# Kernel tuning notes

Hardware: AMD Instinct MI355X
Metric: run time of the kernel (lower is better)

Reference implementation:

```python
import jax, jax.numpy as jnp
import numpy as np

DIM = 512          # model dim
K = 4              # max_block_size (depthwise conv kernel size)
DS = 4             # downsample_factor
BLOCKS = (1, 2, 3, 4)  # block sizes, all offset 0
MULT = 12          # lcm(1,2,3,4) = block_pad_multiple
VOCAB = 256


def setup_inputs() -> dict:
    key = jax.random.key(0)
    ks = jax.random.split(key, 7)
    x = jax.random.randint(ks[0], (4, 4096), 0, VOCAB)
    emb = jax.random.normal(ks[1], (VOCAB, DIM), dtype=jnp.float32) * 0.02
    dw_w = jax.random.normal(ks[2], (DIM, 1, K), dtype=jnp.float32) * 0.1   # depthwise conv weight [out, in/groups, k]
    dw_b = jnp.zeros((DIM,), dtype=jnp.float32)
    pw_w = jax.random.normal(ks[3], (DIM, DIM), dtype=jnp.float32) * 0.05   # 1x1 conv weight [out, in]
    pw_b = jnp.zeros((DIM,), dtype=jnp.float32)
    score_w = jax.random.normal(ks[4], (DIM,), dtype=jnp.float32) * 0.05    # Linear(dim,1)
    score_b = jnp.zeros((), dtype=jnp.float32)
    return {"x": x, "emb": emb, "dw_w": dw_w, "dw_b": dw_b,
            "pw_w": pw_w, "pw_b": pw_b, "score_w": score_w, "score_b": score_b}


def _gbst(x, emb, dw_w, dw_b, pw_w, pw_b, score_w, score_b):
    b, n = x.shape
    m = ((n + DS - 1) // DS) * DS  # next multiple of downsample factor
    xe = emb[x]  # [b, n, d]

    # positional: Pad seq end by K-1, depthwise conv1d(k=K), then 1x1 conv
    xp = jnp.pad(xe, ((0, 0), (0, K - 1), (0, 0)))
    xc = jnp.transpose(xp, (0, 2, 1))  # [b, d, n+K-1]
    y = jax.lax.conv_general_dilated(
        xc, dw_w, window_strides=(1,), padding='VALID',
        dimension_numbers=('NCH', 'OIH', 'NCH'), feature_group_count=DIM)
    y = y + dw_b[None, :, None]                       # [b, d, n]
    y = jnp.einsum('ed,bdn->bne', pw_w, y) + pw_b     # [b, n, d]

    # pad seq to multiple of lcm of block sizes
    L = ((n + MULT - 1) // MULT) * MULT
    xpad = jnp.pad(y, ((0, 0), (0, L - n), (0, 0)))   # [b, L, d]

    # multi-scale block mean pooling, broadcast back to full length
    reprs = []
    for bs in BLOCKS:
        br = xpad.reshape(b, L // bs, bs, DIM).mean(axis=2)  # [b, L/bs, d]
        reprs.append(jnp.repeat(br, bs, axis=1))             # [b, L, d]
    block_reprs = jnp.stack(reprs, axis=2)  # [b, L, nblocks, d]

    # learned block scoring + softmax over block sizes
    scores = jnp.einsum('blkd,d->blk', block_reprs, score_w) + score_b
    scores = jax.nn.softmax(scores, axis=2)  # [b, L, nblocks]

    # consensus attention over positions (inner dim = nblocks)
    sim = jnp.einsum('bik,bjk->bij', scores, scores)  # [b, L, L]
    attn = jax.nn.softmax(sim, axis=-1)
    scores = jnp.einsum('bij,bjk->bik', attn, scores)

    out = jnp.einsum('blkd,blk->bld', block_reprs, scores)  # [b, L, d]
    out = out[:, :m]
    out = out.reshape(b, m // DS, DS, DIM).mean(axis=2)     # [b, m/DS, d]
    return out


def reference(x, emb, dw_w, dw_b, pw_w, pw_b, score_w, score_b):
    return _gbst(x, emb, dw_w, dw_b, pw_w, pw_b, score_w, score_b)
```

## Files before the change

kernel.cpp:

```cpp
#include <hip/hip_runtime.h>
#include <hip/hip_bf16.h>

#define DIMD 512
#define NSEQ 4096
#define LPAD 4104
#define NCH 12
#define CH 342
#define SPLITS 8
#define PT_BK 32

#define OFF_P      0u
#define OFF_CONST  524288u
#define OFF_Q      524800u
#define OFF_S      525824u
#define OFF_AACC   591488u
#define OFF_PPART  657152u

__global__ __launch_bounds__(256) void k_ptable(
    const float* __restrict__ emb, const float* __restrict__ dw_w,
    const float* __restrict__ pw_w, float* __restrict__ Ppart) {
  __shared__ float As[PT_BK][68];
  __shared__ float Bs[PT_BK][68];
  const int tid = threadIdx.x;
  const int m0 = blockIdx.x * 64;
  const int e0 = blockIdx.y * 64;
  const int z  = blockIdx.z;
  const int kk = m0 >> 8;
  const int v0 = m0 & 255;
  const int srow = tid >> 3;
  const int sd4  = (tid & 7) * 4;
  const int ty = tid >> 4, tx = tid & 15;
  float c[4][4] = {};
  for (int kt = 0; kt < 64; kt += PT_BK) {
    const int d0 = z * 64 + kt;
    const float dw0 = dw_w[(d0 + sd4 + 0) * 4 + kk];
    const float dw1 = dw_w[(d0 + sd4 + 1) * 4 + kk];
    const float dw2 = dw_w[(d0 + sd4 + 2) * 4 + kk];
    const float dw3 = dw_w[(d0 + sd4 + 3) * 4 + kk];
    #pragma unroll
    for (int rr = 0; rr < 2; ++rr) {
      const int row = srow + rr * 32;
      float4 ev = *reinterpret_cast<const float4*>(&emb[(v0 + row) * DIMD + d0 + sd4]);
      As[sd4 + 0][row] = ev.x * dw0;
      As[sd4 + 1][row] = ev.y * dw1;
      As[sd4 + 2][row] = ev.z * dw2;
      As[sd4 + 3][row] = ev.w * dw3;
      float4 bv = *reinterpret_cast<const float4*>(&pw_w[(e0 + row) * DIMD + d0 + sd4]);
      Bs[sd4 + 0][row] = bv.x;
      Bs[sd4 + 1][row] = bv.y;
      Bs[sd4 + 2][row] = bv.z;
      Bs[sd4 + 3][row] = bv.w;
    }
    __syncthreads();
    #pragma unroll
    for (int q = 0; q < PT_BK; ++q) {
      float4 a = *reinterpret_cast<const float4*>(&As[q][ty * 4]);
      float4 b = *reinterpret_cast<const float4*>(&Bs[q][tx * 4]);
      c[0][0] += a.x * b.x; c[0][1] += a.x * b.y; c[0][2] += a.x * b.z; c[0][3] += a.x * b.w;
      c[1][0] += a.y * b.x; c[1][1] += a.y * b.y; c[1][2] += a.y * b.z; c[1][3] += a.y * b.w;
      c[2][0] += a.z * b.x; c[2][1] += a.z * b.y; c[2][2] += a.z * b.z; c[2][3] += a.z * b.w;
      c[3][0] += a.w * b.x; c[3][1] += a.w * b.y; c[3][2] += a.w * b.z; c[3][3] += a.w * b.w;
    }
    __syncthreads();
  }
  #pragma unroll
  for (int i = 0; i < 4; ++i) {
    *reinterpret_cast<float4*>(
        &Ppart[(size_t)z * 524288u + (m0 + ty * 4 + i) * DIMD + e0 + tx * 4]) =
        make_float4(c[i][0], c[i][1], c[i][2], c[i][3]);
  }
}

__global__ __launch_bounds__(256) void k_pcomb(
    const float* __restrict__ Ppart, float* __restrict__ P,
    const float* __restrict__ pw_w, const float* __restrict__ pw_b,
    const float* __restrict__ dw_b, const float* __restrict__ score_w,
    float* __restrict__ constv, float* __restrict__ q) {
  __shared__ float qred[4];
  const int tid = threadIdx.x;
  const int idx = blockIdx.x * 256 + tid;
  const float4* p4 = reinterpret_cast<const float4*>(Ppart);
  float4 a = p4[idx];
  #pragma unroll
  for (int zz = 1; zz < SPLITS; ++zz) {
    float4 v = p4[(size_t)zz * 131072u + idx];
    a.x += v.x; a.y += v.y; a.z += v.z; a.w += v.w;
  }
  reinterpret_cast<float4*>(P)[idx] = a;
  float4 sw = reinterpret_cast<const float4*>(score_w)[idx & 127];
  float part = a.x * sw.x + a.y * sw.y + a.z * sw.z + a.w * sw.w;
  for (int off = 32; off > 0; off >>= 1) part += __shfl_down(part, off);
  if ((tid & 63) == 0) qred[tid >> 6] = part;
  __syncthreads();
  if (tid == 0)   q[blockIdx.x * 2 + 0] = qred[0] + qred[1];
  if (tid == 128) q[blockIdx.x * 2 + 1] = qred[2] + qred[3];
  if (blockIdx.x < 2) {
    const int e = blockIdx.x * 256 + tid;
    float acc = pw_b[e];
    const float4* pr = reinterpret_cast<const float4*>(&pw_w[e * DIMD]);
    const float4* db = reinterpret_cast<const float4*>(dw_b);
    for (int d4 = 0; d4 < DIMD / 4; ++d4) {
      float4 w = pr[d4]; float4 bb = db[d4];
      acc += w.x * bb.x + w.y * bb.y + w.z * bb.z + w.w * bb.w;
    }
    constv[e] = acc;
  }
}

__global__ __launch_bounds__(256) void k_scores(
    const int* __restrict__ x, const float* __restrict__ q,
    const float* __restrict__ constv, const float* __restrict__ score_w,
    const float* __restrict__ score_b_p, float* __restrict__ s,
    float* __restrict__ Aacc) {
  __shared__ float qlds[1024];
  __shared__ float tlds[264];
  __shared__ float c0red[2];
  const int b = blockIdx.y;
  const int l0 = blockIdx.x * 256;
  const int tid = threadIdx.x;
  reinterpret_cast<float4*>(qlds)[tid] = reinterpret_cast<const float4*>(q)[tid];
  if (tid < 128) {
    float4 cv = reinterpret_cast<const float4*>(constv)[tid];
    float4 sw = reinterpret_cast<const float4*>(score_w)[tid];
    float part = cv.x * sw.x + cv.y * sw.y + cv.z * sw.z + cv.w * sw.w;
    for (int off = 32; off > 0; off >>= 1) part += __shfl_down(part, off);
    if ((tid & 63) == 0) c0red[tid >> 6] = part;
  }
  __syncthreads();
  const float c0 = c0red[0] + c0red[1];
  const int* xb = &x[b * NSEQ];
  auto tval = [&](int l) -> float {
    if ((unsigned)l >= (unsigned)NSEQ) return 0.f;
    float acc = c0;
    #pragma unroll
    for (int k = 0; k < 4; ++k) {
      const int pos = l + k;
      if (pos < NSEQ) acc += qlds[(k << 8) + xb[pos]];
    }
    return acc;
  };
  tlds[tid] = tval(l0 - 2 + tid);
  if (tid < 5) tlds[256 + tid] = tval(l0 + 254 + tid);
  __syncthreads();
  const int l = l0 + tid;
  if (l >= LPAD) return;
  reinterpret_cast<float4*>(Aacc)[(size_t)(b * LPAD) + l] = make_float4(0.f, 0.f, 0.f, 0.f);
  const float sb = score_b_p[0];
  #define TT(j) tlds[(j) - l0 + 2]
  float p0 = TT(l) + sb;
  int j2 = l & ~1;
  float p1 = (TT(j2) + TT(j2 + 1)) * 0.5f + sb;
  int j3 = (l / 3) * 3;
  float p2 = (TT(j3) + TT(j3 + 1) + TT(j3 + 2)) * (1.0f / 3.0f) + sb;
  int j4 = l & ~3;
  float p3 = (TT(j4) + TT(j4 + 1) + TT(j4 + 2) + TT(j4 + 3)) * 0.25f + sb;
  #undef TT
  float mx = fmaxf(fmaxf(p0, p1), fmaxf(p2, p3));
  float e0 = __expf(p0 - mx), e1 = __expf(p1 - mx);
  float e2 = __expf(p2 - mx), e3 = __expf(p3 - mx);
  float inv = 1.0f / (e0 + e1 + e2 + e3);
  *reinterpret_cast<float4*>(&s[((size_t)(b * LPAD) + l) * 4]) =
      make_float4(e0 * inv, e1 * inv, e2 * inv, e3 * inv);
}

__global__ __launch_bounds__(256) void k_attn(
    const float* __restrict__ s, float* __restrict__ Aacc) {
  const int b = blockIdx.z;
  const int c = blockIdx.y;
  const int i = blockIdx.x * 256 + threadIdx.x;
  __shared__ float4 sch[CH];
  const float4* s4 = reinterpret_cast<const float4*>(s) + (size_t)b * LPAD;
  float4 si = s4[i < LPAD ? i : 0];
  const int j0 = c * CH;
  for (int idx = threadIdx.x; idx < CH; idx += 256) sch[idx] = s4[j0 + idx];
  __syncthreads();
  if (i >= LPAD) return;
  float a0x = 0.f, a0y = 0.f, a0z = 0.f, a0w = 0.f;
  float a1x = 0.f, a1y = 0.f, a1z = 0.f, a1w = 0.f;
  #pragma unroll 3
  for (int jj = 0; jj < CH; jj += 2) {
    float4 u = sch[jj];
    float4 v = sch[jj + 1];
    float d0 = si.x * u.x + si.y * u.y + si.z * u.z + si.w * u.w;
    float d1 = si.x * v.x + si.y * v.y + si.z * v.z + si.w * v.w;
    float e0 = __expf(d0), e1 = __expf(d1);
    a0x += e0 * u.x; a0y += e0 * u.y; a0z += e0 * u.z; a0w += e0 * u.w;
    a1x += e1 * v.x; a1y += e1 * v.y; a1z += e1 * v.z; a1w += e1 * v.w;
  }
  float* aa = &Aacc[((size_t)(b * LPAD) + i) * 4];
  atomicAdd(aa + 0, a0x + a1x);
  atomicAdd(aa + 1, a0y + a1y);
  atomicAdd(aa + 2, a0z + a1z);
  atomicAdd(aa + 3, a0w + a1w);
}

__global__ __launch_bounds__(256) void k_out(
    const int* __restrict__ x, const float* __restrict__ P,
    const float* __restrict__ constv, const float* __restrict__ Aacc,
    float* __restrict__ out) {
  const int b = blockIdx.y;
  const int h = threadIdx.x >> 7;
  const int tl = threadIdx.x & 127;
  const int g = blockIdx.x * 2 + h;
  __shared__ float coef[2][8];
  const int jbase = (g == 0) ? 0 : 4 * g - 2;
  if (tl == 0) {
    float cf[8] = {0.f, 0.f, 0.f, 0.f, 0.f, 0.f, 0.f, 0.f};
    const float4* a4 = reinterpret_cast<const float4*>(Aacc) + (size_t)b * LPAD;
    for (int dl = 0; dl < 4; ++dl) {
      int l = 4 * g + dl;
      float4 av = a4[l];
      float inv = 1.0f / (av.x + av.y + av.z + av.w);
      float sk[4] = {av.x * inv, av.y * inv, av.z * inv, av.w * inv};
      for (int k = 0; k < 4; ++k) {
        int bs = k + 1;
        int j0 = (l / bs) * bs;
        float wv = sk[k] / (float)(bs * 4);
        for (int jj = 0; jj < bs; ++jj) cf[j0 + jj - jbase] += wv;
      }
    }
    for (int r = 0; r < 8; ++r) coef[h][r] = cf[r];
  }
  __syncthreads();
  const int* xb = &x[b * NSEQ];
  float ax = 0.f, ay = 0.f, az = 0.f, aw = 0.f;
  float csum = 0.f;
  #pragma unroll
  for (int r = 0; r < 8; ++r) {
    const int row = jbase + r;
    if (row < NSEQ) {
      const float cr = coef[h][r];
      csum += cr;
      #pragma unroll
      for (int k = 0; k < 4; ++k) {
        const int pos = row + k;
        if (pos < NSEQ) {
          const int tok = xb[pos];
          const float4 pv = *reinterpret_cast<const float4*>(
              &P[((unsigned)(k << 8) + tok) * DIMD + tl * 4]);
          ax += cr * pv.x; ay += cr * pv.y; az += cr * pv.z; aw += cr * pv.w;
        }
      }
    }
  }
  const float4 cv = reinterpret_cast<const float4*>(constv)[tl];
  ax += csum * cv.x; ay += csum * cv.y; az += csum * cv.z; aw += csum * cv.w;
  reinterpret_cast<float4*>(out)[((size_t)(b * 1024) + g) * 128 + tl] =
      make_float4(ax, ay, az, aw);
}

extern "C" void kernel_launch(void* const* d_in, const int* in_sizes, int n_in,
                              void* d_out, int out_size, void* d_ws, size_t ws_size,
                              hipStream_t stream) {
  const int* x = (const int*)d_in[0];
  const float* emb = (const float*)d_in[1];
  const float* dw_w = (const float*)d_in[2];
  const float* dw_b = (const float*)d_in[3];
  const float* pw_w = (const float*)d_in[4];
  const float* pw_b = (const float*)d_in[5];
  const float* score_w = (const float*)d_in[6];
  const float* score_b = (const float*)d_in[7];
  float* out = (float*)d_out;
  float* ws = (float*)d_ws;
  float* P      = ws + OFF_P;
  float* constv = ws + OFF_CONST;
  float* q      = ws + OFF_Q;
  float* s      = ws + OFF_S;
  float* Aacc   = ws + OFF_AACC;
  float* Ppart  = ws + OFF_PPART;

  k_ptable<<<dim3(16, 8, SPLITS), 256, 0, stream>>>(emb, dw_w, pw_w, Ppart);
  k_pcomb<<<512, 256, 0, stream>>>(Ppart, P, pw_w, pw_b, dw_b, score_w, constv, q);
  k_scores<<<dim3(17, 4), 256, 0, stream>>>(x, q, constv, score_w, score_b, s, Aacc);
  k_attn<<<dim3(17, NCH, 4), 256, 0, stream>>>(s, Aacc);
  k_out<<<dim3(512, 4), 256, 0, stream>>>(x, P, constv, Aacc, out);
}
```

Measured before the change: 152.1 us.

## Fuse score computation into attention kernel and batch output groups per block

```diff
diff --git a/kernel.cpp b/kernel.cpp
--- a/kernel.cpp
+++ b/kernel.cpp
@@ -12,9 +12,8 @@
 #define OFF_P      0u
 #define OFF_CONST  524288u
 #define OFF_Q      524800u
-#define OFF_S      525824u
-#define OFF_AACC   591488u
-#define OFF_PPART  657152u
+#define OFF_AACC   525824u
+#define OFF_PPART  591488u
 
 __global__ __launch_bounds__(256) void k_ptable(
     const float* __restrict__ emb, const float* __restrict__ dw_w,
@@ -107,16 +106,19 @@
   }
 }
 
-__global__ __launch_bounds__(256) void k_scores(
+__global__ __launch_bounds__(256) void k_attn(
     const int* __restrict__ x, const float* __restrict__ q,
     const float* __restrict__ constv, const float* __restrict__ score_w,
-    const float* __restrict__ score_b_p, float* __restrict__ s,
-    float* __restrict__ Aacc) {
+    const float* __restrict__ score_b_p, float* __restrict__ Aacc) {
   __shared__ float qlds[1024];
-  __shared__ float tlds[264];
+  __shared__ float tli[264];
+  __shared__ float tlj[348];
+  __shared__ float4 sch[CH];
   __shared__ float c0red[2];
-  const int b = blockIdx.y;
-  const int l0 = blockIdx.x * 256;
+  const int b = blockIdx.z;
+  const int c = blockIdx.y;
+  const int i0 = blockIdx.x * 256;
+  const int j0 = c * CH;
   const int tid = threadIdx.x;
   reinterpret_cast<float4*>(qlds)[tid] = reinterpret_cast<const float4*>(q)[tid];
   if (tid < 128) {
@@ -139,40 +141,46 @@
     }
     return acc;
   };
-  tlds[tid] = tval(l0 - 2 + tid);
-  if (tid < 5) tlds[256 + tid] = tval(l0 + 254 + tid);
-  __syncthreads();
-  const int l = l0 + tid;
-  if (l >= LPAD) return;
-  reinterpret_cast<float4*>(Aacc)[(size_t)(b * LPAD) + l] = make_float4(0.f, 0.f, 0.f, 0.f);
+  for (int idx = tid; idx < 261; idx += 256) tli[idx] = tval(i0 - 2 + idx);
+  for (int idx = tid; idx < 347; idx += 256) tlj[idx] = tval(j0 - 2 + idx);
+  __syncthreads();
   const float sb = score_b_p[0];
-  #define TT(j) tlds[(j) - l0 + 2]
-  float p0 = TT(l) + sb;
-  int j2 = l & ~1;
-  float p1 = (TT(j2) + TT(j2 + 1)) * 0.5f + sb;
-  int j3 = (l / 3) * 3;
-  float p2 = (TT(j3) + TT(j3 + 1) + TT(j3 + 2)) * (1.0f / 3.0f) + sb;
-  int j4 = l & ~3;
-  float p3 = (TT(j4) + TT(j4 + 1) + TT(j4 + 2) + TT(j4 + 3)) * 0.25f + sb;
-  #undef TT
-  float mx = fmaxf(fmaxf(p0, p1), fmaxf(p2, p3));
-  float e0 = __expf(p0 - mx), e1 = __expf(p1 - mx);
-  float e2 = __expf(p2 - mx), e3 = __expf(p3 - mx);
-  float inv = 1.0f / (e0 + e1 + e2 + e3);
-  *reinterpret_cast<float4*>(&s[((size_t)(b * LPAD) + l) * 4]) =
-      make_float4(e0 * inv, e1 * inv, e2 * inv, e3 * inv);
-}
-
-__global__ __launch_bounds__(256) void k_attn(
-    const float* __restrict__ s, float* __restrict__ Aacc) {
-  const int b = blockIdx.z;
-  const int c = blockIdx.y;
-  const int i = blockIdx.x * 256 + threadIdx.x;
-  __shared__ float4 sch[CH];
-  const float4* s4 = reinterpret_cast<const float4*>(s) + (size_t)b * LPAD;
-  float4 si = s4[i < LPAD ? i : 0];
-  const int j0 = c * CH;
-  for (int idx = threadIdx.x; idx < CH; idx += 256) sch[idx] = s4[j0 + idx];
+  for (int idx = tid; idx < CH; idx += 256) {
+    const int l = j0 + idx;
+    #define TJ(j) tlj[(j) - j0 + 2]
+    float p0 = TJ(l) + sb;
+    int j2 = l & ~1;
+    float p1 = (TJ(j2) + TJ(j2 + 1)) * 0.5f + sb;
+    int j3 = (l / 3) * 3;
+    float p2 = (TJ(j3) + TJ(j3 + 1) + TJ(j3 + 2)) * (1.0f / 3.0f) + sb;
+    int j4 = l & ~3;
+    float p3 = (TJ(j4) + TJ(j4 + 1) + TJ(j4 + 2) + TJ(j4 + 3)) * 0.25f + sb;
+    #undef TJ
+    float mx = fmaxf(fmaxf(p0, p1), fmaxf(p2, p3));
+    float e0 = __expf(p0 - mx), e1 = __expf(p1 - mx);
+    float e2 = __expf(p2 - mx), e3 = __expf(p3 - mx);
+    float inv = 1.0f / (e0 + e1 + e2 + e3);
+    sch[idx] = make_float4(e0 * inv, e1 * inv, e2 * inv, e3 * inv);
+  }
+  const int i = i0 + tid;
+  float4 si;
+  {
+    const int l = i;
+    #define TI(j) tli[(j) - i0 + 2]
+    float p0 = TI(l) + sb;
+    int j2 = l & ~1;
+    float p1 = (TI(j2) + TI(j2 + 1)) * 0.5f + sb;
+    int j3 = (l / 3) * 3;
+    float p2 = (TI(j3) + TI(j3 + 1) + TI(j3 + 2)) * (1.0f / 3.0f) + sb;
+    int j4 = l & ~3;
+    float p3 = (TI(j4) + TI(j4 + 1) + TI(j4 + 2) + TI(j4 + 3)) * 0.25f + sb;
+    #undef TI
+    float mx = fmaxf(fmaxf(p0, p1), fmaxf(p2, p3));
+    float e0 = __expf(p0 - mx), e1 = __expf(p1 - mx);
+    float e2 = __expf(p2 - mx), e3 = __expf(p3 - mx);
+    float inv = 1.0f / (e0 + e1 + e2 + e3);
+    si = make_float4(e0 * inv, e1 * inv, e2 * inv, e3 * inv);
+  }
   __syncthreads();
   if (i >= LPAD) return;
   float a0x = 0.f, a0y = 0.f, a0z = 0.f, a0w = 0.f;
@@ -194,59 +202,65 @@
   atomicAdd(aa + 3, a0w + a1w);
 }
 
-__global__ __launch_bounds__(256) void k_out(
+__global__ __launch_bounds__(128) void k_out(
     const int* __restrict__ x, const float* __restrict__ P,
     const float* __restrict__ constv, const float* __restrict__ Aacc,
     float* __restrict__ out) {
   const int b = blockIdx.y;
-  const int h = threadIdx.x >> 7;
-  const int tl = threadIdx.x & 127;
-  const int g = blockIdx.x * 2 + h;
-  __shared__ float coef[2][8];
-  const int jbase = (g == 0) ? 0 : 4 * g - 2;
-  if (tl == 0) {
-    float cf[8] = {0.f, 0.f, 0.f, 0.f, 0.f, 0.f, 0.f, 0.f};
+  const int g0 = blockIdx.x * 4;
+  const int tl = threadIdx.x;
+  const int R0 = 4 * g0 - 2;
+  __shared__ float coef[4][20];
+  if (tl < 80) (&coef[0][0])[tl] = 0.f;
+  __syncthreads();
+  if (tl < 4) {
+    const int g = g0 + tl;
     const float4* a4 = reinterpret_cast<const float4*>(Aacc) + (size_t)b * LPAD;
     for (int dl = 0; dl < 4; ++dl) {
-      int l = 4 * g + dl;
+      const int l = 4 * g + dl;
       float4 av = a4[l];
       float inv = 1.0f / (av.x + av.y + av.z + av.w);
       float sk[4] = {av.x * inv, av.y * inv, av.z * inv, av.w * inv};
       for (int k = 0; k < 4; ++k) {
-        int bs = k + 1;
-        int j0 = (l / bs) * bs;
-        float wv = sk[k] / (float)(bs * 4);
-        for (int jj = 0; jj < bs; ++jj) cf[j0 + jj - jbase] += wv;
+        const int bs = k + 1;
+        const int j0 = (l / bs) * bs;
+        const float wv = sk[k] / (float)(bs * 4);
+        for (int jj = 0; jj < bs; ++jj) coef[tl][j0 + jj - R0] += wv;
       }
     }
-    for (int r = 0; r < 8; ++r) coef[h][r] = cf[r];
   }
   __syncthreads();
   const int* xb = &x[b * NSEQ];
-  float ax = 0.f, ay = 0.f, az = 0.f, aw = 0.f;
-  float csum = 0.f;
-  #pragma unroll
-  for (int r = 0; r < 8; ++r) {
-    const int row = jbase + r;
-    if (row < NSEQ) {
-      const float cr = coef[h][r];
-      csum += cr;
-      #pragma unroll
-      for (int k = 0; k < 4; ++k) {
-        const int pos = row + k;
-        if (pos < NSEQ) {
-          const int tok = xb[pos];
-          const float4 pv = *reinterpret_cast<const float4*>(
-              &P[((unsigned)(k << 8) + tok) * DIMD + tl * 4]);
-          ax += cr * pv.x; ay += cr * pv.y; az += cr * pv.z; aw += cr * pv.w;
-        }
+  const float4 cv = reinterpret_cast<const float4*>(constv)[tl];
+  float4 acc0 = {0.f, 0.f, 0.f, 0.f}, acc1 = {0.f, 0.f, 0.f, 0.f};
+  float4 acc2 = {0.f, 0.f, 0.f, 0.f}, acc3 = {0.f, 0.f, 0.f, 0.f};
+  for (int r = 0; r < 20; ++r) {
+    const int row = R0 + r;
+    if ((unsigned)row >= (unsigned)NSEQ) continue;
+    const float c0 = coef[0][r], c1 = coef[1][r];
+    const float c2 = coef[2][r], c3 = coef[3][r];
+    if (c0 + c1 + c2 + c3 == 0.f) continue;
+    float yx = cv.x, yy = cv.y, yz = cv.z, yw = cv.w;
+    #pragma unroll
+    for (int k = 0; k < 4; ++k) {
+      const int pos = row + k;
+      if (pos < NSEQ) {
+        const int tok = xb[pos];
+        const float4 pv = *reinterpret_cast<const float4*>(
+            &P[((unsigned)(k << 8) + tok) * DIMD + tl * 4]);
+        yx += pv.x; yy += pv.y; yz += pv.z; yw += pv.w;
       }
     }
-  }
-  const float4 cv = reinterpret_cast<const float4*>(constv)[tl];
-  ax += csum * cv.x; ay += csum * cv.y; az += csum * cv.z; aw += csum * cv.w;
-  reinterpret_cast<float4*>(out)[((size_t)(b * 1024) + g) * 128 + tl] =
-      make_float4(ax, ay, az, aw);
+    acc0.x += c0 * yx; acc0.y += c0 * yy; acc0.z += c0 * yz; acc0.w += c0 * yw;
+    acc1.x += c1 * yx; acc1.y += c1 * yy; acc1.z += c1 * yz; acc1.w += c1 * yw;
+    acc2.x += c2 * yx; acc2.y += c2 * yy; acc2.z += c2 * yz; acc2.w += c2 * yw;
+    acc3.x += c3 * yx; acc3.y += c3 * yy; acc3.z += c3 * yz; acc3.w += c3 * yw;
+  }
+  float4* o = reinterpret_cast<float4*>(out) + ((size_t)(b * 1024) + g0) * 128 + tl;
+  o[0 * 128] = acc0;
+  o[1 * 128] = acc1;
+  o[2 * 128] = acc2;
+  o[3 * 128] = acc3;
 }
 
 extern "C" void kernel_launch(void* const* d_in, const int* in_sizes, int n_in,
@@ -265,13 +279,12 @@
   float* P      = ws + OFF_P;
   float* constv = ws + OFF_CONST;
   float* q      = ws + OFF_Q;
-  float* s      = ws + OFF_S;
   float* Aacc   = ws + OFF_AACC;
   float* Ppart  = ws + OFF_PPART;
 
+  hipMemsetAsync(Aacc, 0, (size_t)4 * LPAD * 4 * sizeof(float), stream);
   k_ptable<<<dim3(16, 8, SPLITS), 256, 0, stream>>>(emb, dw_w, pw_w, Ppart);
   k_pcomb<<<512, 256, 0, stream>>>(Ppart, P, pw_w, pw_b, dw_b, score_w, constv, q);
-  k_scores<<<dim3(17, 4), 256, 0, stream>>>(x, q, constv, score_w, score_b, s, Aacc);
-  k_attn<<<dim3(17, NCH, 4), 256, 0, stream>>>(s, Aacc);
-  k_out<<<dim3(512, 4), 256, 0, stream>>>(x, P, constv, Aacc, out);
-}
+  k_attn<<<dim3(17, NCH, 4), 256, 0, stream>>>(x, q, constv, score_w, score_b, Aacc);
+  k_out<<<dim3(256, 4), 128, 0, stream>>>(x, P, constv, Aacc, out);
+}
```

After: 149.3 us. No clear change (-1.9%).
